# Kernel optimization log

Measured on AMD Instinct MI355X. Metric: run time of the kernel, lower is better.

## Reference

```python
import jax, jax.numpy as jnp
import numpy as np

H = 8      # heads
D = 64     # dim_head
DIM = 512  # model dim (== H*D)
LN_EPS = 1e-5


def setup_inputs() -> dict:
    key = jax.random.key(0)
    ks = jax.random.split(key, 4)
    B, N = 8, 1024
    x = jax.random.normal(ks[0], (B, N, DIM), dtype=jnp.float32)
    # params (torch Linear y = x @ W^T; we store W already transposed as (in, out))
    w_qkv = jax.random.normal(ks[1], (DIM, 3 * H * D), dtype=jnp.float32) * (DIM ** -0.5)
    w_out = jax.random.normal(ks[2], (H * D, DIM), dtype=jnp.float32) * ((H * D) ** -0.5)
    b_out = jnp.zeros((DIM,), dtype=jnp.float32)
    ln_g = jnp.ones((DIM,), dtype=jnp.float32)
    ln_b = jnp.zeros((DIM,), dtype=jnp.float32)
    return {"x": x, "w_qkv": w_qkv, "w_out": w_out, "b_out": b_out,
            "ln_g": ln_g, "ln_b": ln_b}


def reference(x, w_qkv, w_out, b_out, ln_g, ln_b):
    b, n, _ = x.shape
    qkv = x @ w_qkv                                   # [b, n, 3*H*D]
    q, k, v = jnp.split(qkv, 3, axis=-1)              # each [b, n, H*D]

    def to_heads(t):                                  # 'b n (h d) -> (b h) n d'
        return t.reshape(b, n, H, D).transpose(0, 2, 1, 3).reshape(b * H, n, D)

    q = to_heads(q)
    k = to_heads(k)
    v = to_heads(v)

    # FAITHFUL to source: k.view(b*h, -1, n) is a row-major reshape, NOT a
    # transpose, and NO scale is applied (self.scale is unused in forward).
    k_r = k.reshape(b * H, D, n)                      # [(bh), D, n] reinterpreted
    dots = jnp.matmul(q, k_r)                          # [(bh), n, n]
    attn = jax.nn.softmax(dots, axis=-1)
    out = jnp.matmul(attn, v)                          # [(bh), n, D]

    # '(b h) n d -> b n (h d)'
    out = out.reshape(b, H, n, D).transpose(0, 2, 1, 3).reshape(b, n, H * D)
    out = out @ w_out + b_out                          # to_out Linear (dropout=0)

    mu = jnp.mean(out, axis=-1, keepdims=True)
    var = jnp.var(out, axis=-1, keepdims=True)
    out = (out - mu) * jax.lax.rsqrt(var + LN_EPS) * ln_g + ln_b
    return out + x
```

## Files before the change

### kernel.cpp

```cpp
#include <hip/hip_runtime.h>

typedef unsigned short u16;
typedef unsigned int u32;
typedef __attribute__((ext_vector_type(4))) float f32x4;
typedef __attribute__((ext_vector_type(8))) short s16x8;

__device__ __forceinline__ u16 bf16_rne(float f) {
    u32 u = __float_as_uint(f);
    u32 r = u + 0x7FFFu + ((u >> 16) & 1u);
    return (u16)(r >> 16);
}

__device__ __forceinline__ u32 cvt_pk_bf16(float lo, float hi) {
    u32 r;
    asm("v_cvt_pk_bf16_f32 %0, %1, %2" : "=v"(r) : "v"(lo), "v"(hi));
    return r;
}

__device__ __forceinline__ void gl_lds16(const void* g, void* l) {
    __builtin_amdgcn_global_load_lds(
        (const __attribute__((address_space(1))) u32*)g,
        (__attribute__((address_space(3))) u32*)l, 16, 0, 0);
}

#define MFMA16(a, b, c) __builtin_amdgcn_mfma_f32_16x16x32_bf16((a), (b), (c), 0, 0, 0)

__global__ __launch_bounds__(256) void k_prep(const float* __restrict__ x,
                                              const float* __restrict__ w_qkv,
                                              const float* __restrict__ w_out,
                                              u16* __restrict__ xbf,
                                              u16* __restrict__ wqkvt,
                                              u16* __restrict__ woutt) {
    const int tid = threadIdx.x;
    if (blockIdx.x < 4096) {
        int i = blockIdx.x * 256 + tid;
        f32x4 v = *(const f32x4*)(x + (size_t)i * 4);
        u32* p = (u32*)(xbf + (size_t)i * 4);
        p[0] = cvt_pk_bf16(v.x, v.y);
        p[1] = cvt_pk_bf16(v.z, v.w);
        return;
    }
    __shared__ float tile[32][33];
    int idx = blockIdx.x - 4096;
    int bx_lin = idx & 63, by4 = idx >> 6;
    const float* in;
    u16* out;
    int C, bxc;
    if (bx_lin < 48) { in = w_qkv; out = wqkvt; C = 1536; bxc = bx_lin; }
    else             { in = w_out; out = woutt; C = 512;  bxc = bx_lin - 48; }
    const int R = 512;
    int bx = bxc * 32;
    int by = by4 * 32;
    int tx = tid & 31;
    int ty = tid >> 5;
#pragma unroll
    for (int i = 0; i < 32; i += 8)
        tile[ty + i][tx] = in[(size_t)(by + ty + i) * C + bx + tx];
    __syncthreads();
#pragma unroll
    for (int i = 0; i < 32; i += 8)
        out[(size_t)(bx + ty + i) * R + by + tx] = bf16_rne(tile[tx][ty + i]);
}

__global__ __launch_bounds__(256) void k_qkv_gemm(
    const u16* __restrict__ xbf, const u16* __restrict__ wt,
    u16* __restrict__ qh, u16* __restrict__ kRT, u16* __restrict__ vT) {
    __shared__ __align__(16) u16 lA[2][128 * 64];
    __shared__ __align__(16) u16 lB[2][128 * 64];
    const int tid = threadIdx.x;
    const int lane = tid & 63, l15 = lane & 15, l4 = lane >> 4;
    const int wid = tid >> 6, wm = wid >> 1, wn = wid & 1;
    const int hw = blockIdx.x;
    const int e = hw & 7, idx = hw >> 3;
    const int m0 = (e + 8 * (idx / 12)) * 128;
    const int c0 = (idx % 12) * 128;

    const char* gA = (const char*)xbf + (size_t)m0 * 1024;
    const char* gB = (const char*)wt + (size_t)c0 * 1024;
    const int srow = tid >> 3;
    const int scol = (tid & 7) * 16;

    const f32x4 z4 = {0.f, 0.f, 0.f, 0.f};
    f32x4 acc[4][4];
#pragma unroll
    for (int i = 0; i < 4; ++i)
#pragma unroll
        for (int j = 0; j < 4; ++j) acc[i][j] = z4;

    auto stage = [&](int buf, int kt) {
#pragma unroll
        for (int q = 0; q < 4; ++q) {
            int row = q * 32 + srow;
            int sc = scol ^ ((row & 7) << 4);
            gl_lds16(gA + (size_t)row * 1024 + kt * 128 + sc,
                     (char*)lA[buf] + q * 4096 + tid * 16);
            gl_lds16(gB + (size_t)row * 1024 + kt * 128 + sc,
                     (char*)lB[buf] + q * 4096 + tid * 16);
        }
    };

    stage(0, 0);
    __syncthreads();
    for (int kt = 0; kt < 8; ++kt) {
        int buf = kt & 1;
        if (kt < 7) stage(buf ^ 1, kt + 1);
        s16x8 af[4][2], bfr[4][2];
#pragma unroll
        for (int i = 0; i < 4; ++i)
#pragma unroll
            for (int k2 = 0; k2 < 2; ++k2) {
                int ra = wm * 64 + i * 16 + l15;
                int ca = (k2 * 64 + l4 * 16) ^ ((ra & 7) << 4);
                af[i][k2] = *(const s16x8*)((const char*)lA[buf] + ra * 128 + ca);
                int rb = wn * 64 + i * 16 + l15;
                int cb = (k2 * 64 + l4 * 16) ^ ((rb & 7) << 4);
                bfr[i][k2] = *(const s16x8*)((const char*)lB[buf] + rb * 128 + cb);
            }
        __builtin_amdgcn_s_setprio(1);
#pragma unroll
        for (int i = 0; i < 4; ++i)
#pragma unroll
            for (int j = 0; j < 4; ++j)
#pragma unroll
                for (int k2 = 0; k2 < 2; ++k2)
                    acc[i][j] = MFMA16(af[i][k2], bfr[j][k2], acc[i][j]);
        __builtin_amdgcn_s_setprio(0);
        __syncthreads();
    }

    char* ct = (char*)lA;
    const int which = c0 >> 9;
    const int hb = (c0 & 511) >> 6;
    const int b = m0 >> 10;
    const int n0 = m0 & 1023;
    const int i4 = (m0 >> 7) & 7;
    const float qsc = (which == 0) ? 1.4426950408889634f : 1.0f;

    if (which != 2) {
#pragma unroll
        for (int i = 0; i < 4; ++i)
#pragma unroll
            for (int j = 0; j < 4; ++j) {
                int col = wn * 64 + j * 16 + l15;
#pragma unroll
                for (int r = 0; r < 4; ++r) {
                    int rr = wm * 64 + i * 16 + l4 * 4 + r;
                    *(u16*)(ct + rr * 256 + ((col * 2) ^ ((rr & 7) << 4))) =
                        bf16_rne(acc[i][j][r] * qsc);
                }
            }
    } else {
#pragma unroll
        for (int i = 0; i < 4; ++i)
#pragma unroll
            for (int j = 0; j < 4; ++j) {
                int col = wn * 64 + j * 16 + l15;
#pragma unroll
                for (int r = 0; r < 4; ++r) {
                    int rr = wm * 64 + i * 16 + l4 * 4 + r;
                    *(u16*)(ct + col * 256 + ((rr * 2) ^ ((col & 7) << 4))) =
                        bf16_rne(acc[i][j][r]);
                }
            }
    }
    __syncthreads();

    if (which == 0) {
#pragma unroll
        for (int p = 0; p < 8; ++p) {
            int cid = p * 256 + tid;
            int row = cid >> 4, sub = cid & 15;
            s16x8 v = *(const s16x8*)(ct + row * 256 + ((sub * 16) ^ ((row & 7) << 4)));
            int bh = b * 8 + hb + (sub >> 3);
            *(s16x8*)((char*)qh + ((size_t)bh * 1024 + n0 + row) * 128 +
                      (sub & 7) * 16) = v;
        }
    } else if (which == 1) {
#pragma unroll
        for (int p = 0; p < 8; ++p) {
            int cid = p * 256 + tid;
            int h = cid >> 10, jb = (cid >> 6) & 15, jd = cid & 63;
            int colb = ((h * 64 + jd) * 2) ^ ((jb & 7) << 4);
            s16x8 v;
#pragma unroll
            for (int ii = 0; ii < 8; ++ii)
                v[ii] = *(const short*)(ct + (jb + ii * 16) * 256 + colb);
            int bh = b * 8 + hb + h;
            *(s16x8*)((char*)kRT + (size_t)bh * 131072 + jb * 8192 + i4 * 1024 +
                      jd * 16) = v;
        }
    } else {
#pragma unroll
        for (int p = 0; p < 8; ++p) {
            int cid = p * 256 + tid;
            int cl = cid >> 4, nc = cid & 15;
            s16x8 v = *(const s16x8*)(ct + cl * 256 + ((nc * 16) ^ ((cl & 7) << 4)));
            int bh = b * 8 + hb + (cl >> 6);
            *(s16x8*)((char*)vT + ((size_t)bh * 64 + (cl & 63)) * 2048 + n0 * 2 +
                      nc * 16) = v;
        }
    }
}

__global__ __launch_bounds__(256) void k_attn(
    const u16* __restrict__ qh, const u16* __restrict__ kRT,
    const u16* __restrict__ vT, u16* __restrict__ attn_out) {
    __shared__ __align__(16) char smem[40960];
    char* qtile = smem;
    char* ktb = smem + 8192;
    char* vtb = smem + 24576;

    const int tid = threadIdx.x;
    const int lane = tid & 63, l15 = lane & 15, l4 = lane >> 4;
    const int wid = tid >> 6;
    const int bh = blockIdx.x, mt = blockIdx.y;

    const char* kb = (const char*)kRT + (size_t)bh * 131072;
    const char* vb = (const char*)vT + (size_t)bh * 64 * 2048;
    const int srow = tid >> 3;
    const int scol = (tid & 7) * 16;

    {
        const char* gq = (const char*)qh + ((size_t)bh * 1024 + mt * 64) * 128;
#pragma unroll
        for (int q = 0; q < 2; ++q) {
            int row = q * 32 + srow;
            int sc = scol ^ ((row & 7) << 4);
            gl_lds16(gq + (size_t)row * 128 + sc, qtile + q * 4096 + tid * 16);
        }
#pragma unroll
        for (int q = 0; q < 2; ++q) {
            int jd = q * 32 + srow;
            int i4s = (tid & 7) ^ (jd & 7);
            gl_lds16(kb + i4s * 1024 + jd * 16, ktb + q * 4096 + tid * 16);
            int sc = scol ^ ((jd & 7) << 4);
            gl_lds16(vb + (size_t)jd * 2048 + sc, vtb + q * 4096 + tid * 16);
        }
    }
    __syncthreads();

    s16x8 qf[2];
#pragma unroll
    for (int k2 = 0; k2 < 2; ++k2) {
        int row = wid * 16 + l15;
        int cq = (k2 * 64 + l4 * 16) ^ ((row & 7) << 4);
        qf[k2] = *(const s16x8*)(qtile + row * 128 + cq);
    }
    __syncthreads();

    char* ptw = smem + wid * 2048;

    const f32x4 z4 = {0.f, 0.f, 0.f, 0.f};
    f32x4 o[4];
    float den = 0.f;
#pragma unroll
    for (int d4 = 0; d4 < 4; ++d4) o[d4] = z4;

    for (int jb = 0; jb < 16; ++jb) {
        const int buf = jb & 1;
        if (jb < 15) {
            int nb = jb + 1, bufn = buf ^ 1;
#pragma unroll
            for (int q = 0; q < 2; ++q) {
                int jd = q * 32 + srow;
                int i4s = (tid & 7) ^ (jd & 7);
                gl_lds16(kb + (size_t)nb * 8192 + i4s * 1024 + jd * 16,
                         ktb + bufn * 8192 + q * 4096 + tid * 16);
                int sc = scol ^ ((jd & 7) << 4);
                gl_lds16(vb + (size_t)jd * 2048 + nb * 128 + sc,
                         vtb + bufn * 8192 + q * 4096 + tid * 16);
            }
        }
        const char* kt = ktb + buf * 8192;
        const char* vt = vtb + buf * 8192;

        s16x8 bk[4][2];
#pragma unroll
        for (int n4 = 0; n4 < 4; ++n4)
#pragma unroll
            for (int k2 = 0; k2 < 2; ++k2) {
                int rn = n4 * 16 + l15;
                int cb = (k2 * 64 + l4 * 16) ^ ((rn & 7) << 4);
                bk[n4][k2] = *(const s16x8*)(kt + rn * 128 + cb);
            }
        f32x4 s[4];
        __builtin_amdgcn_s_setprio(1);
#pragma unroll
        for (int n4 = 0; n4 < 4; ++n4) {
            s[n4] = z4;
#pragma unroll
            for (int k2 = 0; k2 < 2; ++k2)
                s[n4] = MFMA16(bk[n4][k2], qf[k2], s[n4]);
        }
        __builtin_amdgcn_s_setprio(0);

#pragma unroll
        for (int n4 = 0; n4 < 4; ++n4) {
            float e0 = exp2f(s[n4][0]);
            float e1 = exp2f(s[n4][1]);
            float e2 = exp2f(s[n4][2]);
            float e3 = exp2f(s[n4][3]);
            den += (e0 + e1) + (e2 + e3);
            uint2 w;
            w.x = cvt_pk_bf16(e0, e1);
            w.y = cvt_pk_bf16(e2, e3);
            *(uint2*)(ptw + l15 * 128 +
                      ((n4 * 32 + l4 * 8) ^ ((l15 & 7) << 4))) = w;
        }

        s16x8 bv[4][2];
#pragma unroll
        for (int d4 = 0; d4 < 4; ++d4)
#pragma unroll
            for (int k2 = 0; k2 < 2; ++k2) {
                int rn = d4 * 16 + l15;
                int cb = (k2 * 64 + l4 * 16) ^ ((rn & 7) << 4);
                bv[d4][k2] = *(const s16x8*)(vt + rn * 128 + cb);
            }

        s16x8 pa[2];
#pragma unroll
        for (int k2 = 0; k2 < 2; ++k2)
            pa[k2] = *(const s16x8*)(ptw + l15 * 128 +
                                     ((k2 * 64 + l4 * 16) ^ ((l15 & 7) << 4)));

        __builtin_amdgcn_s_setprio(1);
#pragma unroll
        for (int d4 = 0; d4 < 4; ++d4)
#pragma unroll
            for (int k2 = 0; k2 < 2; ++k2)
                o[d4] = MFMA16(bv[d4][k2], pa[k2], o[d4]);
        __builtin_amdgcn_s_setprio(0);

        if (jb < 15) __syncthreads();
    }

    den += __shfl_xor(den, 16);
    den += __shfl_xor(den, 32);
    float inv = 1.0f / den;

    {
        int row = wid * 16 + l15;
        char* ow = smem + row * 128;
#pragma unroll
        for (int d4 = 0; d4 < 4; ++d4) {
            uint2 w;
            w.x = cvt_pk_bf16(o[d4][0] * inv, o[d4][1] * inv);
            w.y = cvt_pk_bf16(o[d4][2] * inv, o[d4][3] * inv);
            *(uint2*)(ow + ((d4 * 32 + l4 * 8) ^ ((row & 7) << 4))) = w;
        }
    }
    __syncthreads();

    {
        char* dst = (char*)attn_out + ((size_t)(bh >> 3) * 1024 + mt * 64) * 1024 +
                    (bh & 7) * 128;
#pragma unroll
        for (int p = 0; p < 2; ++p) {
            int cid = p * 256 + tid;
            int row = cid >> 3, sub = cid & 7;
            s16x8 v = *(const s16x8*)(smem + row * 128 +
                                      ((sub * 16) ^ ((row & 7) << 4)));
            *(s16x8*)(dst + (size_t)row * 1024 + sub * 16) = v;
        }
    }
}

__global__ __launch_bounds__(512) void k_out_ln(
    const u16* __restrict__ aout, const u16* __restrict__ wt,
    const float* __restrict__ bias, const float* __restrict__ x,
    const float* __restrict__ g, const float* __restrict__ bb,
    float* __restrict__ out) {
    __shared__ __align__(16) char smem[131072];
    char* lB[2] = {smem, smem + 65536};
    const int tid = threadIdx.x;
    const int lane = tid & 63, l15 = lane & 15, l4 = lane >> 4;
    const int wid = tid >> 6, wm = wid >> 2, wn = wid & 3;
    const int m0 = blockIdx.x * 32;

    s16x8 af[16];
    {
        const char* arow = (const char*)aout + (size_t)(m0 + wm * 16 + l15) * 1024;
#pragma unroll
        for (int kk = 0; kk < 16; ++kk)
            af[kk] = *(const s16x8*)(arow + kk * 64 + l4 * 16);
    }

    auto stageB = [&](int buf, int kt) {
#pragma unroll
        for (int p = 0; p < 8; ++p) {
            int cid = p * 512 + tid;
            int n = cid >> 3, cc = cid & 7;
            int sc = (cc * 16) ^ ((n & 7) << 4);
            gl_lds16((const char*)wt + (size_t)n * 1024 + kt * 128 + sc,
                     lB[buf] + cid * 16);
        }
    };

    const f32x4 z4 = {0.f, 0.f, 0.f, 0.f};
    f32x4 acc[8];
#pragma unroll
    for (int j = 0; j < 8; ++j) acc[j] = z4;

    stageB(0, 0);
    __syncthreads();
    for (int kt = 0; kt < 8; ++kt) {
        int buf = kt & 1;
        if (kt < 7) stageB(buf ^ 1, kt + 1);
        s16x8 bf2[8][2];
#pragma unroll
        for (int j = 0; j < 8; ++j)
#pragma unroll
            for (int q = 0; q < 2; ++q) {
                int n = wn * 128 + j * 16 + l15;
                int cb = (q * 64 + l4 * 16) ^ ((n & 7) << 4);
                bf2[j][q] = *(const s16x8*)(lB[buf] + n * 128 + cb);
            }
        __builtin_amdgcn_s_setprio(1);
#pragma unroll
        for (int j = 0; j < 8; ++j)
#pragma unroll
            for (int q = 0; q < 2; ++q)
                acc[j] = MFMA16(af[kt * 2 + q], bf2[j][q], acc[j]);
        __builtin_amdgcn_s_setprio(0);
        __syncthreads();
    }

#pragma unroll
    for (int j = 0; j < 8; ++j) {
        int col = wn * 128 + j * 16 + l15;
        float bo = bias[col];
#pragma unroll
        for (int r = 0; r < 4; ++r) {
            int row = wm * 16 + l4 * 4 + r;
            *(float*)(smem + row * 2048 + ((col * 4) ^ ((row & 7) << 4))) =
                acc[j][r] + bo;
        }
    }
    __syncthreads();

    f32x4 g0 = *(const f32x4*)(g + lane * 8);
    f32x4 g1 = *(const f32x4*)(g + lane * 8 + 4);
    f32x4 b0 = *(const f32x4*)(bb + lane * 8);
    f32x4 b1 = *(const f32x4*)(bb + lane * 8 + 4);
#pragma unroll
    for (int rr = 0; rr < 4; ++rr) {
        int row = wid * 4 + rr;
        int sw = (row & 7) << 4;
        f32x4 v0 = *(const f32x4*)(smem + row * 2048 + ((lane * 32) ^ sw));
        f32x4 v1 = *(const f32x4*)(smem + row * 2048 + ((lane * 32 + 16) ^ sw));
        float s = v0.x + v0.y + v0.z + v0.w + v1.x + v1.y + v1.z + v1.w;
        float sq = v0.x * v0.x + v0.y * v0.y + v0.z * v0.z + v0.w * v0.w +
                   v1.x * v1.x + v1.y * v1.y + v1.z * v1.z + v1.w * v1.w;
#pragma unroll
        for (int m = 1; m < 64; m <<= 1) {
            s += __shfl_xor(s, m);
            sq += __shfl_xor(sq, m);
        }
        float mu = s * (1.0f / 512.0f);
        float var = sq * (1.0f / 512.0f) - mu * mu;
        float rstd = rsqrtf(var + 1e-5f);

        const float* xr = x + (size_t)(m0 + row) * 512 + lane * 8;
        f32x4 x0 = *(const f32x4*)(xr);
        f32x4 x1 = *(const f32x4*)(xr + 4);
        f32x4 r0, r1;
#pragma unroll
        for (int u = 0; u < 4; ++u) {
            r0[u] = (v0[u] - mu) * rstd * g0[u] + b0[u] + x0[u];
            r1[u] = (v1[u] - mu) * rstd * g1[u] + b1[u] + x1[u];
        }
        float* orow = out + (size_t)(m0 + row) * 512 + lane * 8;
        *(f32x4*)(orow) = r0;
        *(f32x4*)(orow + 4) = r1;
    }
}

extern "C" void kernel_launch(void* const* d_in, const int* in_sizes, int n_in,
                              void* d_out, int out_size, void* d_ws, size_t ws_size,
                              hipStream_t stream) {
    const float* x = (const float*)d_in[0];
    const float* w_qkv = (const float*)d_in[1];
    const float* w_out = (const float*)d_in[2];
    const float* b_out = (const float*)d_in[3];
    const float* ln_g = (const float*)d_in[4];
    const float* ln_b = (const float*)d_in[5];
    float* out = (float*)d_out;
    char* ws = (char*)d_ws;

    u16* xbf = (u16*)(ws + 0);
    u16* wqkvt = (u16*)(ws + 8388608);
    u16* woutt = (u16*)(ws + 9961472);
    u16* qh = (u16*)(ws + 10485760);
    u16* kRT = (u16*)(ws + 18874368);
    u16* vT = (u16*)(ws + 27262976);
    u16* aout = (u16*)(ws + 35651584);

    k_prep<<<5120, 256, 0, stream>>>(x, w_qkv, w_out, xbf, wqkvt, woutt);
    k_qkv_gemm<<<768, 256, 0, stream>>>(xbf, wqkvt, qh, kRT, vT);
    k_attn<<<dim3(64, 16), 256, 0, stream>>>(qh, kRT, vT, aout);
    k_out_ln<<<256, 512, 0, stream>>>(aout, woutt, b_out, x, ln_g, ln_b, out);
}
```

Before: 82.54 us.

## Load K fragments directly from global into registers with double buffering

The attention kernel no longer stages K tiles through LDS. Each lane loads its MFMA K fragments straight from global memory into registers, prefetching the next block while computing the current one, with the loop manually unrolled by two to alternate the register buffers. This cuts LDS usage from 40 KB to 24 KB and removes the LDS round trip for K, which should help occupancy and LDS bandwidth. In exchange it raises register pressure and exposes global load latency on the critical path.

```diff
diff --git a/kernel.cpp b/kernel.cpp
--- a/kernel.cpp
+++ b/kernel.cpp
@@ -205,10 +205,9 @@
 __global__ __launch_bounds__(256) void k_attn(
     const u16* __restrict__ qh, const u16* __restrict__ kRT,
     const u16* __restrict__ vT, u16* __restrict__ attn_out) {
-    __shared__ __align__(16) char smem[40960];
+    __shared__ __align__(16) char smem[24576];
     char* qtile = smem;
-    char* ktb = smem + 8192;
-    char* vtb = smem + 24576;
+    char* vtb = smem + 8192;
 
     const int tid = threadIdx.x;
     const int lane = tid & 63, l15 = lane & 15, l4 = lane >> 4;
@@ -216,9 +215,11 @@
     const int bh = blockIdx.x, mt = blockIdx.y;
 
     const char* kb = (const char*)kRT + (size_t)bh * 131072;
-    const char* vb = (const char*)vT + (size_t)bh * 64 * 2048;
+    const char* vb = (const char*)vT + (size_t)bh * 131072;
     const int srow = tid >> 3;
     const int scol = (tid & 7) * 16;
+
+    const char* kfb = kb + l4 * 1024 + l15 * 16;
 
     {
         const char* gq = (const char*)qh + ((size_t)bh * 1024 + mt * 64) * 128;
@@ -231,12 +232,16 @@
 #pragma unroll
         for (int q = 0; q < 2; ++q) {
             int jd = q * 32 + srow;
-            int i4s = (tid & 7) ^ (jd & 7);
-            gl_lds16(kb + i4s * 1024 + jd * 16, ktb + q * 4096 + tid * 16);
             int sc = scol ^ ((jd & 7) << 4);
             gl_lds16(vb + (size_t)jd * 2048 + sc, vtb + q * 4096 + tid * 16);
         }
     }
+    s16x8 bkA[4][2], bkB[4][2];
+#pragma unroll
+    for (int n4 = 0; n4 < 4; ++n4)
+#pragma unroll
+        for (int k2 = 0; k2 < 2; ++k2)
+            bkA[n4][k2] = *(const s16x8*)(kfb + k2 * 4096 + n4 * 256);
     __syncthreads();
 
     s16x8 qf[2];
@@ -256,33 +261,26 @@
 #pragma unroll
     for (int d4 = 0; d4 < 4; ++d4) o[d4] = z4;
 
-    for (int jb = 0; jb < 16; ++jb) {
+    auto body = [&](int jb, s16x8 (&bku)[4][2], s16x8 (&bkp)[4][2]) {
         const int buf = jb & 1;
         if (jb < 15) {
+            const char* kn = kfb + (size_t)(jb + 1) * 8192;
+#pragma unroll
+            for (int n4 = 0; n4 < 4; ++n4)
+#pragma unroll
+                for (int k2 = 0; k2 < 2; ++k2)
+                    bkp[n4][k2] = *(const s16x8*)(kn + k2 * 4096 + n4 * 256);
             int nb = jb + 1, bufn = buf ^ 1;
 #pragma unroll
             for (int q = 0; q < 2; ++q) {
                 int jd = q * 32 + srow;
-                int i4s = (tid & 7) ^ (jd & 7);
-                gl_lds16(kb + (size_t)nb * 8192 + i4s * 1024 + jd * 16,
-                         ktb + bufn * 8192 + q * 4096 + tid * 16);
                 int sc = scol ^ ((jd & 7) << 4);
                 gl_lds16(vb + (size_t)jd * 2048 + nb * 128 + sc,
                          vtb + bufn * 8192 + q * 4096 + tid * 16);
             }
         }
-        const char* kt = ktb + buf * 8192;
         const char* vt = vtb + buf * 8192;
 
-        s16x8 bk[4][2];
-#pragma unroll
-        for (int n4 = 0; n4 < 4; ++n4)
-#pragma unroll
-            for (int k2 = 0; k2 < 2; ++k2) {
-                int rn = n4 * 16 + l15;
-                int cb = (k2 * 64 + l4 * 16) ^ ((rn & 7) << 4);
-                bk[n4][k2] = *(const s16x8*)(kt + rn * 128 + cb);
-            }
         f32x4 s[4];
         __builtin_amdgcn_s_setprio(1);
 #pragma unroll
@@ -290,7 +288,7 @@
             s[n4] = z4;
 #pragma unroll
             for (int k2 = 0; k2 < 2; ++k2)
-                s[n4] = MFMA16(bk[n4][k2], qf[k2], s[n4]);
+                s[n4] = MFMA16(bku[n4][k2], qf[k2], s[n4]);
         }
         __builtin_amdgcn_s_setprio(0);
 
@@ -333,6 +331,12 @@
         __builtin_amdgcn_s_setprio(0);
 
         if (jb < 15) __syncthreads();
+    };
+
+#pragma unroll 1
+    for (int jj = 0; jj < 8; ++jj) {
+        body(2 * jj, bkA, bkB);
+        body(2 * jj + 1, bkB, bkA);
     }
 
     den += __shfl_xor(den, 16);
```

After: 90.81 us. +10.0%, slower.

## Rework attention kernel around 32x32 MFMA with register-resident probabilities

Applied to the files above, without the earlier changes.

The attention kernel now gives each block 128 query rows instead of 64, so each K/V tile loaded into shared memory serves twice as many queries. It switches from 16x16x32 to 32x32x16 bf16 MFMA, with each wave owning 32 rows. The exponentiated scores are repacked across lanes with shuffles rather than written to and re-read from shared memory, removing an LDS round trip. In exchange the grid halves to 512 blocks and each thread holds more accumulator registers, which may limit occupancy and latency hiding.

```diff
diff --git a/kernel.cpp b/kernel.cpp
--- a/kernel.cpp
+++ b/kernel.cpp
@@ -3,6 +3,7 @@
 typedef unsigned short u16;
 typedef unsigned int u32;
 typedef __attribute__((ext_vector_type(4))) float f32x4;
+typedef __attribute__((ext_vector_type(16))) float f32x16;
 typedef __attribute__((ext_vector_type(8))) short s16x8;
 
 __device__ __forceinline__ u16 bf16_rne(float f) {
@@ -24,6 +25,9 @@
 }
 
 #define MFMA16(a, b, c) __builtin_amdgcn_mfma_f32_16x16x32_bf16((a), (b), (c), 0, 0, 0)
+#define MFMA32(a, b, c) __builtin_amdgcn_mfma_f32_32x32x16_bf16((a), (b), (c), 0, 0, 0)
+
+union frag_u { u32 u[4]; s16x8 v; };
 
 __global__ __launch_bounds__(256) void k_prep(const float* __restrict__ x,
                                               const float* __restrict__ w_qkv,
@@ -202,59 +206,54 @@
     }
 }
 
-__global__ __launch_bounds__(256) void k_attn(
+__global__ __launch_bounds__(256, 2) void k_attn(
     const u16* __restrict__ qh, const u16* __restrict__ kRT,
     const u16* __restrict__ vT, u16* __restrict__ attn_out) {
-    __shared__ __align__(16) char smem[40960];
+    __shared__ __align__(16) char smem[49152];
     char* qtile = smem;
-    char* ktb = smem + 8192;
-    char* vtb = smem + 24576;
+    char* ktb = smem + 16384;
+    char* vtb = smem + 32768;
 
     const int tid = threadIdx.x;
-    const int lane = tid & 63, l15 = lane & 15, l4 = lane >> 4;
-    const int wid = tid >> 6;
+    const int lane = tid & 63, l31 = lane & 31, sg = lane >> 5;
+    const int wv = tid >> 6;
     const int bh = blockIdx.x, mt = blockIdx.y;
 
     const char* kb = (const char*)kRT + (size_t)bh * 131072;
-    const char* vb = (const char*)vT + (size_t)bh * 64 * 2048;
+    const char* vb = (const char*)vT + (size_t)bh * 131072;
     const int srow = tid >> 3;
     const int scol = (tid & 7) * 16;
 
     {
-        const char* gq = (const char*)qh + ((size_t)bh * 1024 + mt * 64) * 128;
-#pragma unroll
-        for (int q = 0; q < 2; ++q) {
+        const char* gq = (const char*)qh + ((size_t)bh * 1024 + mt * 128) * 128;
+#pragma unroll
+        for (int q = 0; q < 4; ++q) {
             int row = q * 32 + srow;
             int sc = scol ^ ((row & 7) << 4);
             gl_lds16(gq + (size_t)row * 128 + sc, qtile + q * 4096 + tid * 16);
         }
 #pragma unroll
         for (int q = 0; q < 2; ++q) {
-            int jd = q * 32 + srow;
-            int i4s = (tid & 7) ^ (jd & 7);
-            gl_lds16(kb + i4s * 1024 + jd * 16, ktb + q * 4096 + tid * 16);
-            int sc = scol ^ ((jd & 7) << 4);
-            gl_lds16(vb + (size_t)jd * 2048 + sc, vtb + q * 4096 + tid * 16);
-        }
-    }
-    __syncthreads();
-
-    s16x8 qf[2];
-#pragma unroll
-    for (int k2 = 0; k2 < 2; ++k2) {
-        int row = wid * 16 + l15;
-        int cq = (k2 * 64 + l4 * 16) ^ ((row & 7) << 4);
-        qf[k2] = *(const s16x8*)(qtile + row * 128 + cq);
-    }
-    __syncthreads();
-
-    char* ptw = smem + wid * 2048;
-
-    const f32x4 z4 = {0.f, 0.f, 0.f, 0.f};
-    f32x4 o[4];
+            gl_lds16(kb + (q * 256 + tid) * 16, ktb + (q * 256 + tid) * 16);
+            int row = q * 32 + srow;
+            gl_lds16(vb + (size_t)row * 2048 + (scol ^ ((row & 7) << 4)),
+                     vtb + q * 4096 + tid * 16);
+        }
+    }
+    __syncthreads();
+
+    const int qrow = wv * 32 + l31;
+    s16x8 qf[4];
+#pragma unroll
+    for (int iq = 0; iq < 4; ++iq)
+        qf[iq] = *(const s16x8*)(qtile + qrow * 128 +
+                                 ((iq * 32 + sg * 16) ^ ((qrow & 7) << 4)));
+
+    f32x16 zz;
+#pragma unroll
+    for (int r = 0; r < 16; ++r) zz[r] = 0.f;
+    f32x16 o0 = zz, o1 = zz;
     float den = 0.f;
-#pragma unroll
-    for (int d4 = 0; d4 < 4; ++d4) o[d4] = z4;
 
     for (int jb = 0; jb < 16; ++jb) {
         const int buf = jb & 1;
@@ -262,101 +261,105 @@
             int nb = jb + 1, bufn = buf ^ 1;
 #pragma unroll
             for (int q = 0; q < 2; ++q) {
-                int jd = q * 32 + srow;
-                int i4s = (tid & 7) ^ (jd & 7);
-                gl_lds16(kb + (size_t)nb * 8192 + i4s * 1024 + jd * 16,
-                         ktb + bufn * 8192 + q * 4096 + tid * 16);
-                int sc = scol ^ ((jd & 7) << 4);
-                gl_lds16(vb + (size_t)jd * 2048 + nb * 128 + sc,
+                gl_lds16(kb + (size_t)nb * 8192 + (q * 256 + tid) * 16,
+                         ktb + bufn * 8192 + (q * 256 + tid) * 16);
+                int row = q * 32 + srow;
+                gl_lds16(vb + (size_t)row * 2048 + nb * 128 +
+                             (scol ^ ((row & 7) << 4)),
                          vtb + bufn * 8192 + q * 4096 + tid * 16);
             }
         }
         const char* kt = ktb + buf * 8192;
         const char* vt = vtb + buf * 8192;
 
-        s16x8 bk[4][2];
-#pragma unroll
-        for (int n4 = 0; n4 < 4; ++n4)
-#pragma unroll
-            for (int k2 = 0; k2 < 2; ++k2) {
-                int rn = n4 * 16 + l15;
-                int cb = (k2 * 64 + l4 * 16) ^ ((rn & 7) << 4);
-                bk[n4][k2] = *(const s16x8*)(kt + rn * 128 + cb);
-            }
-        f32x4 s[4];
+        f32x16 s0 = zz, s1 = zz;
         __builtin_amdgcn_s_setprio(1);
 #pragma unroll
-        for (int n4 = 0; n4 < 4; ++n4) {
-            s[n4] = z4;
-#pragma unroll
-            for (int k2 = 0; k2 < 2; ++k2)
-                s[n4] = MFMA16(bk[n4][k2], qf[k2], s[n4]);
+        for (int iq = 0; iq < 4; ++iq) {
+            const char* ka = kt + (2 * iq + sg) * 1024 + l31 * 16;
+            s16x8 a0 = *(const s16x8*)(ka);
+            s16x8 a1 = *(const s16x8*)(ka + 512);
+            s0 = MFMA32(a0, qf[iq], s0);
+            s1 = MFMA32(a1, qf[iq], s1);
         }
         __builtin_amdgcn_s_setprio(0);
 
-#pragma unroll
-        for (int n4 = 0; n4 < 4; ++n4) {
-            float e0 = exp2f(s[n4][0]);
-            float e1 = exp2f(s[n4][1]);
-            float e2 = exp2f(s[n4][2]);
-            float e3 = exp2f(s[n4][3]);
-            den += (e0 + e1) + (e2 + e3);
-            uint2 w;
-            w.x = cvt_pk_bf16(e0, e1);
-            w.y = cvt_pk_bf16(e2, e3);
-            *(uint2*)(ptw + l15 * 128 +
-                      ((n4 * 32 + l4 * 8) ^ ((l15 & 7) << 4))) = w;
-        }
-
-        s16x8 bv[4][2];
-#pragma unroll
-        for (int d4 = 0; d4 < 4; ++d4)
-#pragma unroll
-            for (int k2 = 0; k2 < 2; ++k2) {
-                int rn = d4 * 16 + l15;
-                int cb = (k2 * 64 + l4 * 16) ^ ((rn & 7) << 4);
-                bv[d4][k2] = *(const s16x8*)(vt + rn * 128 + cb);
-            }
-
-        s16x8 pa[2];
-#pragma unroll
-        for (int k2 = 0; k2 < 2; ++k2)
-            pa[k2] = *(const s16x8*)(ptw + l15 * 128 +
-                                     ((k2 * 64 + l4 * 16) ^ ((l15 & 7) << 4)));
+        u32 u0[8], u1[8];
+        {
+            f32x16 e0, e1;
+#pragma unroll
+            for (int r = 0; r < 16; ++r) {
+                e0[r] = exp2f(s0[r]);
+                e1[r] = exp2f(s1[r]);
+                den += e0[r] + e1[r];
+            }
+#pragma unroll
+            for (int j = 0; j < 8; ++j) {
+                u0[j] = cvt_pk_bf16(e0[2 * j], e0[2 * j + 1]);
+                u1[j] = cvt_pk_bf16(e1[2 * j], e1[2 * j + 1]);
+            }
+        }
+        s16x8 pa[4];
+        {
+            auto mix = [&](u32 lo, u32 hi, u32& wl, u32& wh) {
+                u32 c = (u32)__shfl_xor((int)(sg ? lo : hi), 32);
+                wl = sg ? c : lo;
+                wh = sg ? hi : c;
+            };
+            frag_u f;
+            mix(u0[0], u0[2], f.u[0], f.u[2]);
+            mix(u0[1], u0[3], f.u[1], f.u[3]);
+            pa[0] = f.v;
+            mix(u0[4], u0[6], f.u[0], f.u[2]);
+            mix(u0[5], u0[7], f.u[1], f.u[3]);
+            pa[1] = f.v;
+            mix(u1[0], u1[2], f.u[0], f.u[2]);
+            mix(u1[1], u1[3], f.u[1], f.u[3]);
+            pa[2] = f.v;
+            mix(u1[4], u1[6], f.u[0], f.u[2]);
+            mix(u1[5], u1[7], f.u[1], f.u[3]);
+            pa[3] = f.v;
+        }
 
         __builtin_amdgcn_s_setprio(1);
 #pragma unroll
-        for (int d4 = 0; d4 < 4; ++d4)
-#pragma unroll
-            for (int k2 = 0; k2 < 2; ++k2)
-                o[d4] = MFMA16(bv[d4][k2], pa[k2], o[d4]);
+        for (int nq = 0; nq < 4; ++nq) {
+            int cb = (nq * 32 + sg * 16) ^ ((l31 & 7) << 4);
+            s16x8 v0 = *(const s16x8*)(vt + l31 * 128 + cb);
+            s16x8 v1 = *(const s16x8*)(vt + (32 + l31) * 128 + cb);
+            o0 = MFMA32(v0, pa[nq], o0);
+            o1 = MFMA32(v1, pa[nq], o1);
+        }
         __builtin_amdgcn_s_setprio(0);
 
         if (jb < 15) __syncthreads();
     }
 
-    den += __shfl_xor(den, 16);
     den += __shfl_xor(den, 32);
     float inv = 1.0f / den;
 
     {
-        int row = wid * 16 + l15;
-        char* ow = smem + row * 128;
-#pragma unroll
-        for (int d4 = 0; d4 < 4; ++d4) {
+        char* ow = smem + qrow * 128;
+        int sw = (qrow & 7) << 4;
+#pragma unroll
+        for (int g = 0; g < 4; ++g) {
             uint2 w;
-            w.x = cvt_pk_bf16(o[d4][0] * inv, o[d4][1] * inv);
-            w.y = cvt_pk_bf16(o[d4][2] * inv, o[d4][3] * inv);
-            *(uint2*)(ow + ((d4 * 32 + l4 * 8) ^ ((row & 7) << 4))) = w;
-        }
-    }
-    __syncthreads();
+            w.x = cvt_pk_bf16(o0[4 * g] * inv, o0[4 * g + 1] * inv);
+            w.y = cvt_pk_bf16(o0[4 * g + 2] * inv, o0[4 * g + 3] * inv);
+            *(uint2*)(ow + ((16 * g + 8 * sg) ^ sw)) = w;
+            w.x = cvt_pk_bf16(o1[4 * g] * inv, o1[4 * g + 1] * inv);
+            w.y = cvt_pk_bf16(o1[4 * g + 2] * inv, o1[4 * g + 3] * inv);
+            *(uint2*)(ow + ((64 + 16 * g + 8 * sg) ^ sw)) = w;
+        }
+    }
+    __syncthreads();
+
 
     {
-        char* dst = (char*)attn_out + ((size_t)(bh >> 3) * 1024 + mt * 64) * 1024 +
+        char* dst = (char*)attn_out + ((size_t)(bh >> 3) * 1024 + mt * 128) * 1024 +
                     (bh & 7) * 128;
 #pragma unroll
-        for (int p = 0; p < 2; ++p) {
+        for (int p = 0; p < 4; ++p) {
             int cid = p * 256 + tid;
             int row = cid >> 3, sub = cid & 7;
             s16x8 v = *(const s16x8*)(smem + row * 128 +
@@ -498,6 +501,6 @@
 
     k_prep<<<5120, 256, 0, stream>>>(x, w_qkv, w_out, xbf, wqkvt, woutt);
     k_qkv_gemm<<<768, 256, 0, stream>>>(xbf, wqkvt, qh, kRT, vT);
-    k_attn<<<dim3(64, 16), 256, 0, stream>>>(qh, kRT, vT, aout);
+    k_attn<<<dim3(64, 8), 256, 0, stream>>>(qh, kRT, vT, aout);
     k_out_ln<<<256, 512, 0, stream>>>(aout, woutt, b_out, x, ln_g, ln_b, out);
 }
```

New measurement: 80.39 us. 1.03x faster.
